# Performance work log

Measured on AMD Instinct MI355X. Metric: run time of the kernel, lower is better.

The kernel has to match this reference:

```python
import jax, jax.numpy as jnp
import numpy as np
from functools import partial

SIGMA = 0.1       # blend_params.sigma (heaviside noise intensity)
GAMMA = 0.1       # blend_params.gamma (argmax noise intensity / z softening)
ZNEAR = 1.0
ZFAR = 100.0
NB_SAMPLES = 4
EPS = 1e-10
N, H, W, K = 8, 256, 256, 8


def random_heaviside(x, noise, sigma):
    # x: (N,H,W,K), noise: (S,N,H,W,K). torch.heaviside(v, ones): 1 for v>=0 else 0.
    maps = (x + sigma * noise >= 0).astype(x.dtype)
    return maps.mean(axis=0)


def random_argmax(z, noise, gamma):
    # z: (N,H,W,Kp), noise: (S,N,H,W,Kp). One-hot of per-sample argmax, averaged.
    zp = z + gamma * noise
    w = jax.nn.one_hot(jnp.argmax(zp, axis=-1), z.shape[-1], dtype=z.dtype)
    return w.mean(axis=0)


def reference(colors, dists, zbuf, pix_to_face, background):
    kh, ka = jax.random.split(jax.random.key(1))
    noise_h = jax.random.normal(kh, (NB_SAMPLES, N, H, W, K), dtype=colors.dtype)
    noise_a = jax.random.normal(ka, (NB_SAMPLES, N, H, W, K + 1), dtype=colors.dtype)

    mask = (pix_to_face >= 0).astype(colors.dtype)          # (N,H,W,K)
    prob_map = random_heaviside(-dists, noise_h, SIGMA) * mask
    alpha = jnp.prod(1.0 - prob_map, axis=-1)               # (N,H,W)

    z_inv = (ZFAR - zbuf) / (ZFAR - ZNEAR) * mask
    z_inv_max = jnp.clip(jnp.max(z_inv, axis=-1, keepdims=True), EPS)
    z_map = jnp.log(EPS + prob_map) + (z_inv - z_inv_max) / GAMMA
    bg_score = jnp.broadcast_to((EPS - z_inv_max) / GAMMA, z_map.shape[:-1] + (1,))
    z_map = jnp.concatenate([z_map, bg_score], axis=-1)     # (N,H,W,K+1)

    randomax = random_argmax(z_map, noise_a, GAMMA)
    wz, wb = randomax[..., :-1], randomax[..., -1:]
    weighted_colors = jnp.einsum('nhwk,nhwkc->nhwc', wz, colors)
    rgb = weighted_colors + wb * background                 # (N,H,W,3)
    a = (1.0 - alpha)[..., None]
    return jnp.concatenate([rgb, a], axis=-1)               # (N,H,W,4)


def setup_inputs() -> dict:
    key = jax.random.key(0)
    k1, k2, k3, k4 = jax.random.split(key, 4)
    colors = jax.random.normal(k1, (N, H, W, K, 3), dtype=jnp.float32)
    dists = jax.random.normal(k2, (N, H, W, K), dtype=jnp.float32)
    zbuf = jax.random.uniform(k3, (N, H, W, K), dtype=jnp.float32)
    pix_to_face = jax.random.randint(k4, (N, H, W, K), 0, 1000)
    background = jnp.ones((3,), dtype=jnp.float32)
    return {"colors": colors, "dists": dists, "zbuf": zbuf,
            "pix_to_face": pix_to_face, "background": background}
```

## Files before the change

kernel.cpp:

```cpp
#include <hip/hip_runtime.h>
#include <cstdint>
#include <cmath>


#pragma clang fp contract(off)

#define NPIX 524288
#define STRIDE_H 4194304u
#define STRIDE_A 4718592u

#define BAND_H 3e-4f
#define BAND_A 5e-5f

__device__ __forceinline__ uint32_t rotl32(uint32_t v, int n) {
  return (v << n) | (v >> (32 - n));
}

__device__ __forceinline__ void tf2x32(uint32_t k0, uint32_t k1,
                                       uint32_t c0, uint32_t c1,
                                       uint32_t& o0, uint32_t& o1) {
  const uint32_t k2 = k0 ^ k1 ^ 0x1BD11BDAu;
  uint32_t x0 = c0 + k0, x1 = c1 + k1;
#define TFR(r) { x0 += x1; x1 = rotl32(x1, r); x1 ^= x0; }
  TFR(13) TFR(15) TFR(26) TFR(6)
  x0 += k1;  x1 += k2 + 1u;
  TFR(17) TFR(29) TFR(16) TFR(24)
  x0 += k2;  x1 += k0 + 2u;
  TFR(13) TFR(15) TFR(26) TFR(6)
  x0 += k0;  x1 += k1 + 3u;
  TFR(17) TFR(29) TFR(16) TFR(24)
  x0 += k1;  x1 += k2 + 4u;
  TFR(13) TFR(15) TFR(26) TFR(6)
  x0 += k2;  x1 += k0 + 5u;
#undef TFR
  o0 = x0; o1 = x1;
}

__device__ __forceinline__ double fast_log(double z) {
  uint64_t b = __double_as_longlong(z);
  int E = (int)(b >> 52) - 1023;
  double m = __longlong_as_double((b & 0x000FFFFFFFFFFFFFULL) |
                                  0x3FF0000000000000ULL);
  bool c = m > 1.4142135623730951;
  m = c ? m * 0.5 : m;
  E = c ? E + 1 : E;
  double d = m + 1.0;
  double r = __builtin_amdgcn_rcp(d);
  r = fma(r, fma(-d, r, 1.0), r);
  r = fma(r, fma(-d, r, 1.0), r);
  double s = (m - 1.0) * r;
  double u = s * s;
  double p = 1.0 / 19.0;
  p = fma(p, u, 1.0 / 17.0);
  p = fma(p, u, 1.0 / 15.0);
  p = fma(p, u, 1.0 / 13.0);
  p = fma(p, u, 1.0 / 11.0);
  p = fma(p, u, 1.0 / 9.0);
  p = fma(p, u, 1.0 / 7.0);
  p = fma(p, u, 1.0 / 5.0);
  p = fma(p, u, 1.0 / 3.0);
  p = fma(p, u, 1.0);
  double lm = (2.0 * s) * p;
  const double LN2_HI = 6.93147180369123816490e-01;
  const double LN2_LO = 1.90821492927058770002e-10;
  double e = (double)E;
  return fma(e, LN2_HI, fma(e, LN2_LO, lm));
}

__device__ __forceinline__ float normal_exact(uint32_t bits) {
  float f = __uint_as_float((bits >> 9) | 0x3f800000u) - 1.0f;
  const float lo = __uint_as_float(0xBF7FFFFFu);
  float v = __fadd_rn(__fmul_rn(f, 2.0f), lo);
  v = fmaxf(lo, v);
  float t = -__fmul_rn(v, v);
  float taylor = __fmul_rn(__fadd_rn(__fmul_rn(-0.5f, t), 1.0f), t);
  float lg = (float)fast_log((double)__fadd_rn(t, 1.0f));
  float l1p = (fabsf(t) < 1e-4f) ? taylor : lg;
  float w = -l1p;
  const bool lt = w < 5.0f;
  float ww = lt ? __fsub_rn(w, 2.5f) : __fsub_rn(__fsqrt_rn(w), 3.0f);
  float p  = lt ? 2.81022636e-08f : -0.000200214257f;
  p = __fadd_rn(lt ?  3.43273939e-07f :  0.000100950558f, __fmul_rn(p, ww));
  p = __fadd_rn(lt ? -3.5233877e-06f  :  0.00134934322f,  __fmul_rn(p, ww));
  p = __fadd_rn(lt ? -4.39150654e-06f : -0.00367342844f,  __fmul_rn(p, ww));
  p = __fadd_rn(lt ?  0.00021858087f  :  0.00573950773f,  __fmul_rn(p, ww));
  p = __fadd_rn(lt ? -0.00125372503f  : -0.0076224613f,   __fmul_rn(p, ww));
  p = __fadd_rn(lt ? -0.00417768164f  :  0.00943887047f,  __fmul_rn(p, ww));
  p = __fadd_rn(lt ?  0.246640727f    :  1.00167406f,     __fmul_rn(p, ww));
  p = __fadd_rn(lt ?  1.50140941f     :  2.83297682f,     __fmul_rn(p, ww));
  return __fmul_rn(__uint_as_float(0x3FB504F3u), __fmul_rn(p, v));
}

__device__ __forceinline__ float normal_fast(uint32_t bits) {
  float f = __uint_as_float((bits >> 9) | 0x3f800000u) - 1.0f;
  const float lo = __uint_as_float(0xBF7FFFFFu);
  float v = __fadd_rn(__fmul_rn(f, 2.0f), lo);
  v = fmaxf(lo, v);
  float t = -__fmul_rn(v, v);
  float u = __fadd_rn(t, 1.0f);
  float wlog = __fmul_rn(-0.6931471805599453f, __builtin_amdgcn_logf(u));
  float wtay = __fmul_rn(__fmaf_rn(0.5f, t, -1.0f), t);
  float w = (fabsf(t) < 1e-4f) ? wtay : wlog;
  float ww = w - 2.5f;
  float p = 2.81022636e-08f;
  p = __fmaf_rn(p, ww,  3.43273939e-07f);
  p = __fmaf_rn(p, ww, -3.5233877e-06f);
  p = __fmaf_rn(p, ww, -4.39150654e-06f);
  p = __fmaf_rn(p, ww,  0.00021858087f);
  p = __fmaf_rn(p, ww, -0.00125372503f);
  p = __fmaf_rn(p, ww, -0.00417768164f);
  p = __fmaf_rn(p, ww,  0.246640727f);
  p = __fmaf_rn(p, ww,  1.50140941f);
  if (__builtin_expect(__ballot(w >= 5.0f) != 0ull, 0)) {
    float w2 = __builtin_amdgcn_sqrtf(w) - 3.0f;
    float q = -0.000200214257f;
    q = __fmaf_rn(q, w2,  0.000100950558f);
    q = __fmaf_rn(q, w2,  0.00134934322f);
    q = __fmaf_rn(q, w2, -0.00367342844f);
    q = __fmaf_rn(q, w2,  0.00573950773f);
    q = __fmaf_rn(q, w2, -0.0076224613f);
    q = __fmaf_rn(q, w2,  0.00943887047f);
    q = __fmaf_rn(q, w2,  1.00167406f);
    q = __fmaf_rn(q, w2,  2.83297682f);
    p = (w < 5.0f) ? p : q;
  }
  return __fmul_rn(1.4142135f, __fmul_rn(p, v));
}

__global__ __launch_bounds__(256) void RandomPhongShader_kernel(
    const float* __restrict__ colors,
    const float* __restrict__ dists,
    const float* __restrict__ zbuf,
    const int*   __restrict__ p2f,
    const float* __restrict__ bg,
    float* __restrict__ out)
{
  __shared__ float zmS[256][9];
  const int tid = threadIdx.x;
  const int P = blockIdx.x * 256 + tid;
  if (P >= NPIX) return;

  uint32_t kh0, kh1, ka0, ka1;
  tf2x32(0u, 1u, 0u, 0u, kh0, kh1);
  tf2x32(0u, 1u, 0u, 1u, ka0, ka1);

  float vs[8];
  {
    const float4* d4 = reinterpret_cast<const float4*>(dists + (size_t)P * 8);
    float4 a = d4[0], b = d4[1];
    float dk[8] = {a.x,a.y,a.z,a.w,b.x,b.y,b.z,b.w};
    #pragma unroll
    for (int k = 0; k < 8; ++k) {
      float y = fabsf(dk[k]) * 7.0710678f;
      float tt = __builtin_amdgcn_rcpf(__fmaf_rn(0.3275911f, y, 1.0f));
      float ex = __builtin_amdgcn_exp2f(__fmul_rn(-1.4426951f, y * y));
      float pp = 1.061405429f;
      pp = __fmaf_rn(pp, tt, -1.453152027f);
      pp = __fmaf_rn(pp, tt,  1.421413741f);
      pp = __fmaf_rn(pp, tt, -0.284496736f);
      pp = __fmaf_rn(pp, tt,  0.254829592f);
      float er = __fmaf_rn(-pp * tt, ex, 1.0f);
      vs[k] = copysignf(er, dk[k]);
    }
  }

  const float lo = __uint_as_float(0xBF7FFFFFu);
  uint32_t cntP = 0;
  uint32_t cH = (uint32_t)P * 8u;
  #pragma unroll 1
  for (int s = 0; s < 4; ++s) {
    uint32_t fm = 0, dm = 0;
    #pragma unroll
    for (int k = 0; k < 8; ++k) {
      uint32_t o0, o1;
      tf2x32(kh0, kh1, 0u, cH + (uint32_t)k, o0, o1);
      uint32_t bits = o0 ^ o1;
      float f = __uint_as_float((bits >> 9) | 0x3f800000u) - 1.0f;
      float vapp = __fmaf_rn(f, 2.0f, lo);
      bool de = vapp >= vs[k];
      fm |= (fabsf(vapp - vs[k]) < BAND_H ? 1u : 0u) << k;
      dm |= (de ? 1u : 0u) << k;
      cntP += de ? (1u << (4 * k)) : 0u;
    }
    if (__builtin_expect(fm != 0u, 0)) {
      #pragma unroll 1
      for (int k = 0; k < 8; ++k) {
        if ((fm >> k) & 1u) {
          uint32_t o0, o1;
          tf2x32(kh0, kh1, 0u, cH + (uint32_t)k, o0, o1);
          float nz = normal_exact(o0 ^ o1);
          float x = -dists[(size_t)P * 8 + k];
          uint32_t ed = (__fadd_rn(x, __fmul_rn(0.1f, nz)) >= 0.0f) ? 1u : 0u;
          cntP += (ed - ((dm >> k) & 1u)) << (4 * k);
        }
      }
    }
    cH += STRIDE_H;
  }

  float zk[8];
  int mk[8];
  {
    const float4* z4 = reinterpret_cast<const float4*>(zbuf + (size_t)P * 8);
    float4 c = z4[0], e = z4[1];
    zk[0]=c.x; zk[1]=c.y; zk[2]=c.z; zk[3]=c.w; zk[4]=e.x; zk[5]=e.y; zk[6]=e.z; zk[7]=e.w;
    const int4* m4 = reinterpret_cast<const int4*>(p2f + (size_t)P * 8);
    int4 f = m4[0], g = m4[1];
    mk[0]=f.x; mk[1]=f.y; mk[2]=f.z; mk[3]=f.w; mk[4]=g.x; mk[5]=g.y; mk[6]=g.z; mk[7]=g.w;
  }
  float zinv[8], zmax;
  #pragma unroll
  for (int k = 0; k < 8; ++k) {
    const float m = (mk[k] >= 0) ? 1.0f : 0.0f;
    float zi = __fmul_rn(__fdiv_rn(__fsub_rn(100.0f, zk[k]), 99.0f), m);
    zinv[k] = zi;
    zmax = (k == 0) ? zi : fmaxf(zmax, zi);
  }
  zmax = fmaxf(zmax, 1e-10f);

  const float lg0 = (float)-23.025850916589025;
  const float lg1 = (float)-1.3862943611198906;
  const float lg2 = (float)-0.6931471805599453;
  const float lg3 = (float)-0.2876820724517809;

  float alpha = 1.0f;
  float zm[9];
  #pragma unroll
  for (int k = 0; k < 8; ++k) {
    const int cntk = (int)((cntP >> (4 * k)) & 15u);
    const float m = (mk[k] >= 0) ? 1.0f : 0.0f;
    const float pm = __fmul_rn(__fmul_rn((float)cntk, 0.25f), m);
    alpha *= (1.0f - pm);
    const int i = (mk[k] >= 0) ? cntk : 0;
    const float lg = (i == 0) ? lg0 : (i == 1) ? lg1 : (i == 2) ? lg2
                   : (i == 3) ? lg3 : 0.0f;
    zm[k] = __fadd_rn(lg, __fdiv_rn(__fsub_rn(zinv[k], zmax), 0.1f));
    zmS[tid][k] = zm[k];
  }
  zm[8] = __fdiv_rn(__fsub_rn(1e-10f, zmax), 0.1f);
  zmS[tid][8] = zm[8];

  uint32_t amPack = 0;
  uint32_t cA = (uint32_t)P * 9u;
  #pragma unroll 1
  for (int s = 0; s < 4; ++s) {
    int am = 0;
    float best = -3.4e38f;
    bool fl = false;
    #pragma unroll
    for (int j = 0; j < 9; ++j) {
      uint32_t o0, o1;
      tf2x32(ka0, ka1, 0u, cA + (uint32_t)j, o0, o1);
      float nz = normal_fast(o0 ^ o1);
      float vv = __fmaf_rn(0.1f, nz, zm[j]);
      fl |= fabsf(vv - best) < BAND_A;
      bool g = vv > best;
      best = g ? vv : best;
      am = g ? j : am;
    }
    if (__builtin_expect(__ballot(fl) != 0ull, 0)) {
      if (fl) {
        int ame = 0;
        float be = -3.4e38f;
        #pragma unroll 1
        for (int j = 0; j < 9; ++j) {
          uint32_t o0, o1;
          tf2x32(ka0, ka1, 0u, cA + (uint32_t)j, o0, o1);
          float nz = normal_exact(o0 ^ o1);
          float ve = __fadd_rn(zmS[tid][j], __fmul_rn(0.1f, nz));
          bool g = ve > be;
          be = g ? ve : be;
          ame = g ? j : ame;
        }
        am = ame;
      }
    }
    amPack += 1u << (3 * am);
    cA += STRIDE_A;
  }

  float wgt[9];
  #pragma unroll
  for (int j = 0; j < 9; ++j)
    wgt[j] = __fmul_rn(0.25f, (float)((amPack >> (3 * j)) & 7u));

  float cc[24];
  {
    const float4* c4 = reinterpret_cast<const float4*>(colors + (size_t)P * 24);
    #pragma unroll
    for (int q = 0; q < 6; ++q) {
      float4 t = c4[q];
      cc[q*4+0]=t.x; cc[q*4+1]=t.y; cc[q*4+2]=t.z; cc[q*4+3]=t.w;
    }
  }
  float rgb[3];
  #pragma unroll
  for (int c = 0; c < 3; ++c) {
    float acc = 0.0f;
    #pragma unroll
    for (int k = 0; k < 8; ++k)
      acc = __fadd_rn(acc, __fmul_rn(wgt[k], cc[k * 3 + c]));
    rgb[c] = __fadd_rn(acc, __fmul_rn(wgt[8], bg[c]));
  }

  float4 o;
  o.x = rgb[0]; o.y = rgb[1]; o.z = rgb[2];
  o.w = __fsub_rn(1.0f, alpha);
  reinterpret_cast<float4*>(out)[P] = o;
}

extern "C" void kernel_launch(void* const* d_in, const int* in_sizes, int n_in,
                              void* d_out, int out_size, void* d_ws, size_t ws_size,
                              hipStream_t stream) {
  const float* colors = (const float*)d_in[0];
  const float* dists  = (const float*)d_in[1];
  const float* zbuf   = (const float*)d_in[2];
  const int*   p2f    = (const int*)d_in[3];
  const float* bg     = (const float*)d_in[4];
  float* out = (float*)d_out;
  dim3 grid(NPIX / 256), block(256);
  hipLaunchKernelGGL(RandomPhongShader_kernel, grid, block, 0, stream,
                     colors, dists, zbuf, p2f, bg, out);
}
```

Baseline: 196.0 us.

## Use integer mantissa thresholds for heaviside test and top-two gap for argmax band

The heaviside pass now compares the raw 23-bit uniform mantissa against a per-k integer threshold computed once from erf. The exact normal is recomputed for the whole pixel (wave-level ballot) only when a sample falls within a few ulps of that threshold. The argmax pass folds the noise scaling and zm add into one fma, tracks best and second-best to decide when to fall back, drops shared memory staging, and replaces fp32 divisions with double multiplies. These cut per-sample ALU work and LDS traffic, at the risk of correctness near the thresholds and a larger divergent fallback when one is taken.

```diff
diff --git a/kernel.cpp b/kernel.cpp
--- a/kernel.cpp
+++ b/kernel.cpp
@@ -8,8 +8,6 @@
 #define NPIX 524288
 #define STRIDE_H 4194304u
 #define STRIDE_A 4718592u
-
-#define BAND_H 3e-4f
 #define BAND_A 5e-5f
 
 __device__ __forceinline__ uint32_t rotl32(uint32_t v, int n) {
@@ -91,17 +89,14 @@
   return __fmul_rn(__uint_as_float(0x3FB504F3u), __fmul_rn(p, v));
 }
 
-__device__ __forceinline__ float normal_fast(uint32_t bits) {
+__device__ __forceinline__ float score_fast(uint32_t bits, float zmj) {
   float f = __uint_as_float((bits >> 9) | 0x3f800000u) - 1.0f;
   const float lo = __uint_as_float(0xBF7FFFFFu);
-  float v = __fadd_rn(__fmul_rn(f, 2.0f), lo);
-  v = fmaxf(lo, v);
+  float v = fmaxf(lo, __fmaf_rn(f, 2.0f, lo));
   float t = -__fmul_rn(v, v);
   float u = __fadd_rn(t, 1.0f);
-  float wlog = __fmul_rn(-0.6931471805599453f, __builtin_amdgcn_logf(u));
-  float wtay = __fmul_rn(__fmaf_rn(0.5f, t, -1.0f), t);
-  float w = (fabsf(t) < 1e-4f) ? wtay : wlog;
-  float ww = w - 2.5f;
+  float L = __builtin_amdgcn_logf(u);
+  float ww = __fmaf_rn(-0.69314718f, L, -2.5f);
   float p = 2.81022636e-08f;
   p = __fmaf_rn(p, ww,  3.43273939e-07f);
   p = __fmaf_rn(p, ww, -3.5233877e-06f);
@@ -111,7 +106,8 @@
   p = __fmaf_rn(p, ww, -0.00417768164f);
   p = __fmaf_rn(p, ww,  0.246640727f);
   p = __fmaf_rn(p, ww,  1.50140941f);
-  if (__builtin_expect(__ballot(w >= 5.0f) != 0ull, 0)) {
+  if (__builtin_expect(__ballot(L <= -7.2134752f) != 0ull, 0)) {
+    float w = __fmul_rn(-0.69314718f, L);
     float w2 = __builtin_amdgcn_sqrtf(w) - 3.0f;
     float q = -0.000200214257f;
     q = __fmaf_rn(q, w2,  0.000100950558f);
@@ -122,9 +118,9 @@
     q = __fmaf_rn(q, w2,  0.00943887047f);
     q = __fmaf_rn(q, w2,  1.00167406f);
     q = __fmaf_rn(q, w2,  2.83297682f);
-    p = (w < 5.0f) ? p : q;
-  }
-  return __fmul_rn(1.4142135f, __fmul_rn(p, v));
+    p = (L <= -7.2134752f) ? q : p;
+  }
+  return __fmaf_rn(__fmul_rn(p, v), 0.14142136f, zmj);
 }
 
 __global__ __launch_bounds__(256) void RandomPhongShader_kernel(
@@ -135,72 +131,19 @@
     const float* __restrict__ bg,
     float* __restrict__ out)
 {
-  __shared__ float zmS[256][9];
   const int tid = threadIdx.x;
   const int P = blockIdx.x * 256 + tid;
-  if (P >= NPIX) return;
 
   uint32_t kh0, kh1, ka0, ka1;
   tf2x32(0u, 1u, 0u, 0u, kh0, kh1);
   tf2x32(0u, 1u, 0u, 1u, ka0, ka1);
 
-  float vs[8];
+  float dk[8], zk[8];
+  int mk[8];
   {
     const float4* d4 = reinterpret_cast<const float4*>(dists + (size_t)P * 8);
     float4 a = d4[0], b = d4[1];
-    float dk[8] = {a.x,a.y,a.z,a.w,b.x,b.y,b.z,b.w};
-    #pragma unroll
-    for (int k = 0; k < 8; ++k) {
-      float y = fabsf(dk[k]) * 7.0710678f;
-      float tt = __builtin_amdgcn_rcpf(__fmaf_rn(0.3275911f, y, 1.0f));
-      float ex = __builtin_amdgcn_exp2f(__fmul_rn(-1.4426951f, y * y));
-      float pp = 1.061405429f;
-      pp = __fmaf_rn(pp, tt, -1.453152027f);
-      pp = __fmaf_rn(pp, tt,  1.421413741f);
-      pp = __fmaf_rn(pp, tt, -0.284496736f);
-      pp = __fmaf_rn(pp, tt,  0.254829592f);
-      float er = __fmaf_rn(-pp * tt, ex, 1.0f);
-      vs[k] = copysignf(er, dk[k]);
-    }
-  }
-
-  const float lo = __uint_as_float(0xBF7FFFFFu);
-  uint32_t cntP = 0;
-  uint32_t cH = (uint32_t)P * 8u;
-  #pragma unroll 1
-  for (int s = 0; s < 4; ++s) {
-    uint32_t fm = 0, dm = 0;
-    #pragma unroll
-    for (int k = 0; k < 8; ++k) {
-      uint32_t o0, o1;
-      tf2x32(kh0, kh1, 0u, cH + (uint32_t)k, o0, o1);
-      uint32_t bits = o0 ^ o1;
-      float f = __uint_as_float((bits >> 9) | 0x3f800000u) - 1.0f;
-      float vapp = __fmaf_rn(f, 2.0f, lo);
-      bool de = vapp >= vs[k];
-      fm |= (fabsf(vapp - vs[k]) < BAND_H ? 1u : 0u) << k;
-      dm |= (de ? 1u : 0u) << k;
-      cntP += de ? (1u << (4 * k)) : 0u;
-    }
-    if (__builtin_expect(fm != 0u, 0)) {
-      #pragma unroll 1
-      for (int k = 0; k < 8; ++k) {
-        if ((fm >> k) & 1u) {
-          uint32_t o0, o1;
-          tf2x32(kh0, kh1, 0u, cH + (uint32_t)k, o0, o1);
-          float nz = normal_exact(o0 ^ o1);
-          float x = -dists[(size_t)P * 8 + k];
-          uint32_t ed = (__fadd_rn(x, __fmul_rn(0.1f, nz)) >= 0.0f) ? 1u : 0u;
-          cntP += (ed - ((dm >> k) & 1u)) << (4 * k);
-        }
-      }
-    }
-    cH += STRIDE_H;
-  }
-
-  float zk[8];
-  int mk[8];
-  {
+    dk[0]=a.x; dk[1]=a.y; dk[2]=a.z; dk[3]=a.w; dk[4]=b.x; dk[5]=b.y; dk[6]=b.z; dk[7]=b.w;
     const float4* z4 = reinterpret_cast<const float4*>(zbuf + (size_t)P * 8);
     float4 c = z4[0], e = z4[1];
     zk[0]=c.x; zk[1]=c.y; zk[2]=c.z; zk[3]=c.w; zk[4]=e.x; zk[5]=e.y; zk[6]=e.z; zk[7]=e.w;
@@ -208,11 +151,70 @@
     int4 f = m4[0], g = m4[1];
     mk[0]=f.x; mk[1]=f.y; mk[2]=f.z; mk[3]=f.w; mk[4]=g.x; mk[5]=g.y; mk[6]=g.z; mk[7]=g.w;
   }
+
+  int Tm6[8];
+  #pragma unroll
+  for (int k = 0; k < 8; ++k) {
+    float y = fabsf(dk[k]) * 7.0710678f;
+    float tt = __builtin_amdgcn_rcpf(__fmaf_rn(0.3275911f, y, 1.0f));
+    float ex = __builtin_amdgcn_exp2f(__fmul_rn(-1.4426951f, y * y));
+    float pp = 1.061405429f;
+    pp = __fmaf_rn(pp, tt, -1.453152027f);
+    pp = __fmaf_rn(pp, tt,  1.421413741f);
+    pp = __fmaf_rn(pp, tt, -0.284496736f);
+    pp = __fmaf_rn(pp, tt,  0.254829592f);
+    float er = __fmaf_rn(-pp * tt, ex, 1.0f);
+    float vs = copysignf(er, dk[k]);
+    int T = (int)ceilf(__fmul_rn(__fadd_rn(vs, 0.99999994f), 4194304.0f));
+    Tm6[k] = T - 6;
+  }
+
+  uint32_t cntP = 0;
+  bool redoH = false;
+  {
+    uint32_t cH = (uint32_t)P * 8u;
+    #pragma unroll 1
+    for (int s = 0; s < 4; ++s) {
+      #pragma unroll
+      for (int k = 0; k < 8; ++k) {
+        uint32_t o0, o1;
+        tf2x32(kh0, kh1, 0u, cH + (uint32_t)k, o0, o1);
+        int m = (int)((o0 ^ o1) >> 9);
+        int sub = m - Tm6[k];
+        cntP += (sub >= 6) ? (1u << (4 * k)) : 0u;
+        redoH |= ((uint32_t)sub <= 12u);
+      }
+      cH += STRIDE_H;
+    }
+  }
+  if (__builtin_expect(__ballot(redoH) != 0ull, 0)) {
+    if (redoH) {
+      uint32_t c2 = 0;
+      uint32_t cH = (uint32_t)P * 8u;
+      #pragma unroll 1
+      for (int s = 0; s < 4; ++s) {
+        #pragma unroll 1
+        for (int k = 0; k < 8; ++k) {
+          uint32_t o0, o1;
+          tf2x32(kh0, kh1, 0u, cH + (uint32_t)k, o0, o1);
+          float nz = normal_exact(o0 ^ o1);
+          float x = -dists[(size_t)P * 8 + k];
+          c2 += (__fadd_rn(x, __fmul_rn(0.1f, nz)) >= 0.0f) ? (1u << (4 * k)) : 0u;
+        }
+        cH += STRIDE_H;
+      }
+      cntP = c2;
+    }
+  }
+
+  const double D99 = 1.0 / 99.0;
+  const double D01 = 1.0 / (double)0.1f;
   float zinv[8], zmax;
   #pragma unroll
   for (int k = 0; k < 8; ++k) {
     const float m = (mk[k] >= 0) ? 1.0f : 0.0f;
-    float zi = __fmul_rn(__fdiv_rn(__fsub_rn(100.0f, zk[k]), 99.0f), m);
+    float a = __fsub_rn(100.0f, zk[k]);
+    float zi = __fmul_rn((float)((double)a * D99), m);
     zinv[k] = zi;
     zmax = (k == 0) ? zi : fmaxf(zmax, zi);
   }
@@ -234,40 +236,38 @@
     const int i = (mk[k] >= 0) ? cntk : 0;
     const float lg = (i == 0) ? lg0 : (i == 1) ? lg1 : (i == 2) ? lg2
                    : (i == 3) ? lg3 : 0.0f;
-    zm[k] = __fadd_rn(lg, __fdiv_rn(__fsub_rn(zinv[k], zmax), 0.1f));
-    zmS[tid][k] = zm[k];
-  }
-  zm[8] = __fdiv_rn(__fsub_rn(1e-10f, zmax), 0.1f);
-  zmS[tid][8] = zm[8];
+    float sdf = __fsub_rn(zinv[k], zmax);
+    zm[k] = __fadd_rn(lg, (float)((double)sdf * D01));
+  }
+  zm[8] = (float)((double)__fsub_rn(1e-10f, zmax) * D01);
 
   uint32_t amPack = 0;
   uint32_t cA = (uint32_t)P * 9u;
   #pragma unroll 1
   for (int s = 0; s < 4; ++s) {
     int am = 0;
-    float best = -3.4e38f;
-    bool fl = false;
+    float best = -3.4e38f, second = -3.4e38f;
     #pragma unroll
     for (int j = 0; j < 9; ++j) {
       uint32_t o0, o1;
       tf2x32(ka0, ka1, 0u, cA + (uint32_t)j, o0, o1);
-      float nz = normal_fast(o0 ^ o1);
-      float vv = __fmaf_rn(0.1f, nz, zm[j]);
-      fl |= fabsf(vv - best) < BAND_A;
+      float vv = score_fast(o0 ^ o1, zm[j]);
       bool g = vv > best;
+      second = g ? best : fmaxf(second, vv);
       best = g ? vv : best;
       am = g ? j : am;
     }
+    bool fl = __fsub_rn(best, second) < BAND_A;
     if (__builtin_expect(__ballot(fl) != 0ull, 0)) {
       if (fl) {
         int ame = 0;
         float be = -3.4e38f;
-        #pragma unroll 1
+        #pragma unroll
         for (int j = 0; j < 9; ++j) {
           uint32_t o0, o1;
           tf2x32(ka0, ka1, 0u, cA + (uint32_t)j, o0, o1);
           float nz = normal_exact(o0 ^ o1);
-          float ve = __fadd_rn(zmS[tid][j], __fmul_rn(0.1f, nz));
+          float ve = __fadd_rn(zm[j], __fmul_rn(0.1f, nz));
           bool g = ve > be;
           be = g ? ve : be;
           ame = g ? j : ame;
```

Measured after the change: 201.6 us. 1.03x slower.
